# Optimization experiments

Measured on AMD Instinct MI355X. Metric: run time of the kernel, lower is better.

Reference implementation:

```python
import jax, jax.numpy as jnp
import numpy as np

B, H, S, D = 2, 12, 4096, 64
BLK = 64              # from_block_size == to_block_size
NB = S // BLK         # 64 blocks
R = 3                 # num_rand_blocks
NEG = -10000.0


def setup_inputs() -> dict:
    key = jax.random.key(0)
    kq, kk, kv, kr = jax.random.split(key, 4)
    f32 = jnp.float32
    return dict(
        query_layer=jax.random.normal(kq, (B, H, S, D), dtype=f32),
        key_layer=jax.random.normal(kk, (B, H, S, D), dtype=f32),
        value_layer=jax.random.normal(kv, (B, H, S, D), dtype=f32),
        band_mask=jnp.ones((B, 1, NB - 4, BLK, 3 * BLK), dtype=f32),
        from_mask=jnp.ones((B, 1, S, 1), dtype=f32),
        to_mask=jnp.ones((B, 1, 1, S), dtype=f32),
        from_blocked_mask=jnp.ones((B, NB, BLK), dtype=f32),
        to_blocked_mask=jnp.ones((B, NB, BLK), dtype=f32),
        rand_attn=jax.random.randint(kr, (B, H, NB - 2, R), 1, NB - 1, dtype=jnp.int32),
    )


def reference(query_layer, key_layer, value_layer, band_mask, from_mask, to_mask,
              from_blocked_mask, to_blocked_mask, rand_attn):
    b, h, f, d = query_layer.shape
    t = key_layer.shape[2]
    wm = band_mask.shape[3]          # from block size
    wn = band_mask.shape[4] // 3     # to block size
    nf, nt = f // wm, t // wn
    r = rand_attn.shape[-1]
    scale = 1.0 / np.sqrt(d).astype(np.float32)
    softmax = lambda x: jax.nn.softmax(x, axis=-1)

    bq = query_layer.reshape(b, h, nf, wm, d)
    bk = key_layer.reshape(b, h, nt, wn, d)
    bv = value_layer.reshape(b, h, nt, wn, d)

    # gather random key/value blocks: [b,h,nf-2,r*wn,d]
    idx = rand_attn.reshape(b, h, (nf - 2) * r, 1, 1)
    gk = jnp.take_along_axis(bk, idx, axis=2).reshape(b, h, nf - 2, r * wn, d)
    gv = jnp.take_along_axis(bv, idx, axis=2).reshape(b, h, nf - 2, r * wn, d)

    # random attention mask: [b,h,nf-2,wm,r*wn]
    rm = jax.vmap(lambda m, i: m[i])(to_blocked_mask, rand_attn)  # [b,h,nf-2,r,wn]
    rm = rm.reshape(b, h, nf - 2, r * wn)
    rand_mask = jnp.einsum('blq,bhlk->bhlqk', from_blocked_mask[:, 1:-1], rm)

    # --- first query block: dense attention over all keys ---
    fp = jnp.einsum('bhqd,bhkd->bhqk', bq[:, :, 0], key_layer) * scale
    fp = fp + (1.0 - to_mask) * NEG
    first_ctx = jnp.einsum('bhqk,bhkd->bhqd', softmax(fp), value_layer)[:, :, None]

    # --- second query block: blocks 0,1,2, last, random ---
    sk = jnp.concatenate([bk[:, :, 0], bk[:, :, 1], bk[:, :, 2], bk[:, :, -1], gk[:, :, 0]], axis=2)
    sv = jnp.concatenate([bv[:, :, 0], bv[:, :, 1], bv[:, :, 2], bv[:, :, -1], gv[:, :, 0]], axis=2)
    sp = jnp.einsum('bhqd,bhkd->bhqk', bq[:, :, 1], sk) * scale
    seq_pad = jnp.concatenate([to_mask[:, :, :, :3 * wn], to_mask[:, :, :, -wn:],
                               jnp.ones((b, 1, 1, r * wn), dtype=to_mask.dtype)], axis=3)
    rnd_pad = jnp.concatenate([jnp.ones((b, h, wm, 4 * wn), dtype=rand_mask.dtype),
                               rand_mask[:, :, 0]], axis=3)
    sp = sp + (1.0 - jnp.minimum(seq_pad, rnd_pad)) * NEG
    second_ctx = jnp.einsum('bhqk,bhkd->bhqd', softmax(sp), sv)[:, :, None]

    # --- middle blocks: sliding window + random + 2 global ---
    exp_k = jnp.concatenate([bk[:, :, 1:-3], bk[:, :, 2:-2], bk[:, :, 3:-1]], axis=3)
    exp_v = jnp.concatenate([bv[:, :, 1:-3], bv[:, :, 2:-2], bv[:, :, 3:-1]], axis=3)
    mq = bq[:, :, 2:-2]
    inner = jnp.einsum('bhlqd,bhlkd->bhlqk', mq, exp_k) * scale + (1.0 - band_mask) * NEG
    randp = jnp.einsum('bhlqd,bhlkd->bhlqk', mq, gk[:, :, 1:-1]) * scale \
            + (1.0 - rand_mask[:, :, 1:-1]) * NEG
    firstp = jnp.einsum('bhlqd,bhkd->bhlqk', mq, bk[:, :, 0]) * scale \
             + (1.0 - to_mask[:, :, :, :wn][:, :, :, None, :]) * NEG
    lastp = jnp.einsum('bhlqd,bhkd->bhlqk', mq, bk[:, :, -1]) * scale \
            + (1.0 - to_mask[:, :, :, -wn:][:, :, :, None, :]) * NEG
    band = jnp.concatenate([firstp, inner, randp, lastp], axis=-1)
    aw = softmax(band)
    ctx = jnp.einsum('bhlqk,bhlkd->bhlqd', aw[..., wn:4 * wn], exp_v)
    ctx = ctx + jnp.einsum('bhlqk,bhlkd->bhlqd', aw[..., 4 * wn:-wn], gv[:, :, 1:-1])
    ctx = ctx + jnp.einsum('bhlqk,bhkd->bhlqd', aw[..., :wn], bv[:, :, 0])
    ctx = ctx + jnp.einsum('bhlqk,bhkd->bhlqd', aw[..., -wn:], bv[:, :, -1])

    # --- second-to-last query block ---
    slk = jnp.concatenate([bk[:, :, 0], bk[:, :, -3], bk[:, :, -2], bk[:, :, -1], gk[:, :, -1]], axis=2)
    slv = jnp.concatenate([bv[:, :, 0], bv[:, :, -3], bv[:, :, -2], bv[:, :, -1], gv[:, :, -1]], axis=2)
    slp = jnp.einsum('bhqd,bhkd->bhqk', bq[:, :, -2], slk) * scale
    seq_pad2 = jnp.concatenate([to_mask[:, :, :, :wn], to_mask[:, :, :, -3 * wn:],
                                jnp.ones((b, 1, 1, r * wn), dtype=to_mask.dtype)], axis=3)
    rnd_pad2 = jnp.concatenate([jnp.ones((b, h, wm, 4 * wn), dtype=rand_mask.dtype),
                                rand_mask[:, :, -1]], axis=3)
    slp = slp + (1.0 - jnp.minimum(seq_pad2, rnd_pad2)) * NEG
    second_last_ctx = jnp.einsum('bhqk,bhkd->bhqd', softmax(slp), slv)[:, :, None]

    # --- last query block: dense attention over all keys ---
    lp = jnp.einsum('bhqd,bhkd->bhqk', bq[:, :, -1], key_layer) * scale
    lp = lp + (1.0 - to_mask) * NEG
    last_ctx = jnp.einsum('bhqk,bhkd->bhqd', softmax(lp), value_layer)[:, :, None]

    out = jnp.concatenate([first_ctx, second_ctx, ctx, second_last_ctx, last_ctx], axis=2)
    out = out.reshape(b, h, f, d) * from_mask
    return jnp.transpose(out, (0, 2, 1, 3))  # [b, f, h, d]
```

## Files before the change

### kernel.cpp

```cpp
#include <hip/hip_runtime.h>
#include <math.h>

#define PS 4224
#define NEG -10000.f

typedef short short8v __attribute__((ext_vector_type(8)));
typedef float f32x4  __attribute__((ext_vector_type(4)));

#define KHo  0
#define KLo  4096
#define VTHo 8192
#define VTLo 12288
#define LDS_TOT 16384

__device__ __forceinline__ unsigned au(float x){ return __float_as_uint(x); }
__device__ __forceinline__ float    af(unsigned x){ return __uint_as_float(x); }

__device__ __forceinline__ void pack4(float a, float b, float c, float d,
                                      unsigned &h01, unsigned &h23,
                                      unsigned &l01, unsigned &l23) {
    unsigned u0=au(a), u1=au(b), u2=au(c), u3=au(d);
    h01 = __builtin_amdgcn_perm(u1, u0, 0x07060302);
    h23 = __builtin_amdgcn_perm(u3, u2, 0x07060302);
    float r0 = a - af(u0 & 0xffff0000u);
    float r1 = b - af(u1 & 0xffff0000u);
    float r2 = c - af(u2 & 0xffff0000u);
    float r3 = d - af(u3 & 0xffff0000u);
    l01 = __builtin_amdgcn_perm(au(r1), au(r0), 0x07060302);
    l23 = __builtin_amdgcn_perm(au(r3), au(r2), 0x07060302);
}

__device__ __forceinline__ int swz(int row, int colus) {
    return row*64 + (((colus>>3) ^ (row&7))<<3) + (colus&7);
}

#define MFMA(a,b,c) __builtin_amdgcn_mfma_f32_16x16x32_bf16((a),(b),(c),0,0,0)

union FragU { unsigned u[4]; short8v s; };

__device__ __forceinline__ void tile_of(bool partial, bool isMid, int m, int seg,
                                        int r0, int r1, int r2i, int t,
                                        int &blk, int &ty) {
    if (partial)     { blk = seg*8 + t; ty = 0; }
    else if (isMid) {
        if (t == 0)      { blk = 0;       ty = 0; }
        else if (t <= 3) { blk = m-2 + t; ty = t; }
        else if (t <= 6) { blk = (t==4)?r0:((t==5)?r1:r2i); ty = 4; }
        else             { blk = 63;      ty = 0; }
    } else {
        if (t < 4) { blk = (m==1) ? ((t<3)? t : 63) : ((t==0)? 0 : 60+t); ty = 0; }
        else       { blk = (t==4)?r0:((t==5)?r1:r2i); ty = 4; }
    }
}

__global__ __launch_bounds__(256, 3) void bigbird_attn(
    const float* __restrict__ Qg, const float* __restrict__ Kg, const float* __restrict__ Vg,
    const float* __restrict__ band_mask, const float* __restrict__ from_mask,
    const float* __restrict__ to_mask, const float* __restrict__ fbm,
    const float* __restrict__ tbm, const int* __restrict__ rand_attn,
    float* __restrict__ out, float* __restrict__ ws)
{
    const int H = 12, S = 4096;
    __shared__ __align__(16) unsigned short lds[LDS_TOT];

    const int tid  = threadIdx.x;
    const int w    = tid >> 6;
    const int lane = tid & 63;
    const int l15  = lane & 15;
    const int l4   = lane >> 4;

    int wg = blockIdx.x;
    int b, h, m, seg = 0;
    bool partial;
    if (wg < 384) {
        partial = true;
        b = wg / 192;
        int r = wg - b*192;
        h = r >> 4;
        int r2 = r & 15;
        m = (r2 >> 3) ? 63 : 0;
        seg = r2 & 7;
    } else {
        partial = false;
        int ww = wg - 384;
        b = ww / (H*62);
        int r = ww - b*H*62;
        h = r / 62;
        m = 1 + (r - h*62);
    }

    const long bh = (long)b*H + h;
    const float* Qb = Qg + (bh*S + (long)m*64)*64;
    const float* Kb = Kg + bh*S*64;
    const float* Vb = Vg + bh*S*64;

    const bool isMid = (m >= 2) && (m <= 61);
    int nt_cnt;
    int r0 = 1, r1 = 1, r2i = 1;
    if (partial) nt_cnt = 8;
    else {
        const int* ra = rand_attn + (bh*62 + (m-1))*3;
        r0 = ra[0]; r1 = ra[1]; r2i = ra[2];
        nt_cnt = isMid ? 8 : 7;
    }

    short8v qhf[2], qlf[2];
    #pragma unroll
    for (int ks = 0; ks < 2; ++ks) {
        const float* qp = &Qb[(16*w + l15)*64 + l4*8 + 32*ks];
        float4 a = *(const float4*)qp;
        float4 b2 = *(const float4*)(qp + 4);
        FragU fh, fl;
        pack4(a.x,a.y,a.z,a.w, fh.u[0],fh.u[1], fl.u[0],fl.u[1]);
        pack4(b2.x,b2.y,b2.z,b2.w, fh.u[2],fh.u[3], fl.u[2],fl.u[3]);
        qhf[ks] = fh.s; qlf[ks] = fl.s;
    }

    const int kr0 = tid >> 4;
    const int kc  = (tid & 15) << 2;
    const int vd  = tid & 63;
    const int vkg = tid >> 6;

    int blkN, tyN;
    tile_of(partial, isMid, m, seg, r0, r1, r2i, 0, blkN, tyN);
    float4 kreg[4];
    float  vreg[16];
    {
        const float* Kt = Kb + (long)blkN*4096;
        const float* Vt0 = Vb + (long)blkN*4096;
        #pragma unroll
        for (int c = 0; c < 4; ++c) kreg[c] = *(const float4*)&Kt[(kr0+16*c)*64 + kc];
        #pragma unroll
        for (int p = 0; p < 4; ++p)
            #pragma unroll
            for (int i = 0; i < 4; ++i)
                vreg[p*4+i] = Vt0[(p*16 + vkg*4 + i)*64 + vd];
    }

    f32x4 oacc[4];
    #pragma unroll
    for (int i = 0; i < 4; ++i) oacc[i] = (f32x4){0.f,0.f,0.f,0.f};
    float mrow = -INFINITY, lrow = 0.f;

    for (int t = 0; t < nt_cnt; ++t) {
        const int blk = blkN, ty = tyN;

        __syncthreads();

        #pragma unroll
        for (int c = 0; c < 4; ++c) {
            FragU fh, fl;
            pack4(kreg[c].x,kreg[c].y,kreg[c].z,kreg[c].w, fh.u[0],fh.u[1], fl.u[0],fl.u[1]);
            int o = swz(kr0+16*c, kc);
            *(uint2*)&lds[KHo + o] = make_uint2(fh.u[0],fh.u[1]);
            *(uint2*)&lds[KLo + o] = make_uint2(fl.u[0],fl.u[1]);
        }
        #pragma unroll
        for (int p = 0; p < 4; ++p) {
            FragU fh, fl;
            pack4(vreg[p*4+0],vreg[p*4+1],vreg[p*4+2],vreg[p*4+3],
                  fh.u[0],fh.u[1], fl.u[0],fl.u[1]);
            int o = swz(vd, p*16 + vkg*4);
            *(uint2*)&lds[VTHo + o] = make_uint2(fh.u[0],fh.u[1]);
            *(uint2*)&lds[VTLo + o] = make_uint2(fl.u[0],fl.u[1]);
        }
        __syncthreads();

        if (t + 1 < nt_cnt) {
            tile_of(partial, isMid, m, seg, r0, r1, r2i, t+1, blkN, tyN);
            const float* Kt = Kb + (long)blkN*4096;
            const float* Vt0 = Vb + (long)blkN*4096;
            #pragma unroll
            for (int c = 0; c < 4; ++c) kreg[c] = *(const float4*)&Kt[(kr0+16*c)*64 + kc];
            #pragma unroll
            for (int p = 0; p < 4; ++p)
                #pragma unroll
                for (int i = 0; i < 4; ++i)
                    vreg[p*4+i] = Vt0[(p*16 + vkg*4 + i)*64 + vd];
        }

        f32x4 addv[4];
        if (ty == 0) {
            #pragma unroll
            for (int nt = 0; nt < 4; ++nt) {
                f32x4 tv = *(const f32x4*)&to_mask[(long)b*S + blk*64 + 16*nt + 4*l4];
                addv[nt] = (1.f - tv) * NEG;
            }
        } else if (ty <= 3) {
            const float* bq = band_mask + ((long)(b*60 + (m-2)))*64*192
                              + (16*w + l15)*192 + (ty-1)*64;
            #pragma unroll
            for (int nt = 0; nt < 4; ++nt) {
                f32x4 tv = *(const f32x4*)&bq[16*nt + 4*l4];
                addv[nt] = (1.f - tv) * NEG;
            }
        } else {
            float fq = fbm[((long)b*64 + m)*64 + 16*w + l15];
            #pragma unroll
            for (int nt = 0; nt < 4; ++nt) {
                f32x4 tv = *(const f32x4*)&tbm[((long)b*64 + blk)*64 + 16*nt + 4*l4];
                addv[nt] = (1.f - fq*tv) * NEG;
            }
        }

        f32x4 sacc[4];
        #pragma unroll
        for (int nt = 0; nt < 4; ++nt) sacc[nt] = (f32x4){0.f,0.f,0.f,0.f};
        #pragma unroll
        for (int ks = 0; ks < 2; ++ks) {
            const int col = l4*8 + 32*ks;
            #pragma unroll
            for (int nt = 0; nt < 4; ++nt) {
                int o = swz(16*nt + l15, col);
                short8v kh = *(const short8v*)&lds[KHo + o];
                short8v kl = *(const short8v*)&lds[KLo + o];
                sacc[nt] = MFMA(kh, qhf[ks], sacc[nt]);
                sacc[nt] = MFMA(kl, qhf[ks], sacc[nt]);
                sacc[nt] = MFMA(kh, qlf[ks], sacc[nt]);
            }
        }

        f32x4 sr[4];
        float mx = -INFINITY;
        #pragma unroll
        for (int nt = 0; nt < 4; ++nt) {
            sr[nt] = sacc[nt]*0.125f + addv[nt];
            mx = fmaxf(mx, fmaxf(fmaxf(sr[nt][0], sr[nt][1]), fmaxf(sr[nt][2], sr[nt][3])));
        }
        mx = fmaxf(mx, __shfl_xor(mx, 16));
        mx = fmaxf(mx, __shfl_xor(mx, 32));
        float mn = fmaxf(mrow, mx);
        float al = __expf(mrow - mn);
        float ls = 0.f;
        f32x4 pq[4];
        #pragma unroll
        for (int nt = 0; nt < 4; ++nt) {
            pq[nt][0] = __expf(sr[nt][0] - mn);
            pq[nt][1] = __expf(sr[nt][1] - mn);
            pq[nt][2] = __expf(sr[nt][2] - mn);
            pq[nt][3] = __expf(sr[nt][3] - mn);
            ls += pq[nt][0] + pq[nt][1] + pq[nt][2] + pq[nt][3];
        }
        ls += __shfl_xor(ls, 16);
        ls += __shfl_xor(ls, 32);
        lrow = lrow*al + ls;
        mrow = mn;

        unsigned ph01[4], ph23[4], pl01[4], pl23[4];
        #pragma unroll
        for (int nt = 0; nt < 4; ++nt)
            pack4(pq[nt][0],pq[nt][1],pq[nt][2],pq[nt][3],
                  ph01[nt],ph23[nt], pl01[nt],pl23[nt]);

        short8v pbh[2], pbl[2];
        #pragma unroll
        for (int ks = 0; ks < 2; ++ks) {
            const int loNT = 2*ks, hiNT = 2*ks+1;
            const bool up = (l4 & 2);
            unsigned aH0 = up ? ph01[hiNT] : ph01[loNT];
            unsigned aH1 = up ? ph23[hiNT] : ph23[loNT];
            unsigned aL0 = up ? pl01[hiNT] : pl01[loNT];
            unsigned aL1 = up ? pl23[hiNT] : pl23[loNT];
            unsigned sH0 = up ? ph01[loNT] : ph01[hiNT];
            unsigned sH1 = up ? ph23[loNT] : ph23[hiNT];
            unsigned sL0 = up ? pl01[loNT] : pl01[hiNT];
            unsigned sL1 = up ? pl23[loNT] : pl23[hiNT];
            unsigned x16H0 = __shfl_xor((int)aH0, 16), x16H1 = __shfl_xor((int)aH1, 16);
            unsigned x16L0 = __shfl_xor((int)aL0, 16), x16L1 = __shfl_xor((int)aL1, 16);
            unsigned x32H0 = __shfl_xor((int)sH0, 32), x32H1 = __shfl_xor((int)sH1, 32);
            unsigned x32L0 = __shfl_xor((int)sL0, 32), x32L1 = __shfl_xor((int)sL1, 32);
            unsigned x48H0 = __shfl_xor((int)sH0, 48), x48H1 = __shfl_xor((int)sH1, 48);
            unsigned x48L0 = __shfl_xor((int)sL0, 48), x48L1 = __shfl_xor((int)sL1, 48);
            FragU fh, fl;
            fh.u[0] = (l4==0)?aH0 : (l4==1)?x48H0 : (l4==2)?x32H0 : x16H0;
            fh.u[1] = (l4==0)?aH1 : (l4==1)?x48H1 : (l4==2)?x32H1 : x16H1;
            fh.u[2] = (l4==0)?x16H0 : (l4==1)?x32H0 : (l4==2)?x48H0 : aH0;
            fh.u[3] = (l4==0)?x16H1 : (l4==1)?x32H1 : (l4==2)?x48H1 : aH1;
            fl.u[0] = (l4==0)?aL0 : (l4==1)?x48L0 : (l4==2)?x32L0 : x16L0;
            fl.u[1] = (l4==0)?aL1 : (l4==1)?x48L1 : (l4==2)?x32L1 : x16L1;
            fl.u[2] = (l4==0)?x16L0 : (l4==1)?x32L0 : (l4==2)?x48L0 : aL0;
            fl.u[3] = (l4==0)?x16L1 : (l4==1)?x32L1 : (l4==2)?x48L1 : aL1;
            pbh[ks] = fh.s; pbl[ks] = fl.s;
        }

        #pragma unroll
        for (int dnt = 0; dnt < 4; ++dnt) oacc[dnt] *= al;
        #pragma unroll
        for (int ks = 0; ks < 2; ++ks) {
            const int col = l4*8 + 32*ks;
            #pragma unroll
            for (int dnt = 0; dnt < 4; ++dnt) {
                int o = swz(16*dnt + l15, col);
                short8v vh = *(const short8v*)&lds[VTHo + o];
                short8v vl = *(const short8v*)&lds[VTLo + o];
                oacc[dnt] = MFMA(vh, pbh[ks], oacc[dnt]);
                oacc[dnt] = MFMA(vl, pbh[ks], oacc[dnt]);
                oacc[dnt] = MFMA(vh, pbl[ks], oacc[dnt]);
            }
        }
    }

    const int q64 = 16*w + l15;
    if (partial) {
        float* P = ws + ((bh*2 + (m ? 1 : 0))*8 + seg) * PS;
        #pragma unroll
        for (int dnt = 0; dnt < 4; ++dnt)
            *(f32x4*)&P[q64*64 + 16*dnt + 4*l4] = oacc[dnt];
        if (l4 == 0) { P[4096 + q64] = mrow; P[4160 + q64] = lrow; }
    } else {
        int qg = m*64 + q64;
        float scn = (1.f / lrow) * from_mask[(long)b*S + qg];
        #pragma unroll
        for (int dnt = 0; dnt < 4; ++dnt) {
            f32x4 o = oacc[dnt] * scn;
            *(f32x4*)&out[((long)((long)b*S + qg)*H + h)*64 + 16*dnt + 4*l4] = o;
        }
    }
}

__global__ __launch_bounds__(256) void bigbird_reduce(
    const float* __restrict__ ws, const float* __restrict__ from_mask,
    float* __restrict__ out)
{
    const int H = 12, S = 4096;
    int rowIdx = blockIdx.x;
    int b  = rowIdx / 24;
    int r  = rowIdx - b*24;
    int h  = r >> 1;
    int mi = r & 1;
    int m  = mi ? 63 : 0;

    const float* base = ws + (long)rowIdx * 8 * PS;
    int tid = threadIdx.x;
    int q  = tid >> 2;
    int dd = (tid & 3) << 4;

    float msg[8], lsg[8];
    float M = -INFINITY;
    #pragma unroll
    for (int s = 0; s < 8; ++s) {
        msg[s] = base[s*PS + 4096 + q];
        lsg[s] = base[s*PS + 4160 + q];
        M = fmaxf(M, msg[s]);
    }
    float L = 0.f, wv[8];
    #pragma unroll
    for (int s = 0; s < 8; ++s) { wv[s] = __expf(msg[s] - M); L += wv[s]*lsg[s]; }

    int qg = m*64 + q;
    float sc = from_mask[(long)b*S + qg] / L;

    #pragma unroll
    for (int c = 0; c < 4; ++c) {
        float4 o = make_float4(0.f, 0.f, 0.f, 0.f);
        #pragma unroll
        for (int s = 0; s < 8; ++s) {
            float4 a = *(const float4*)&base[s*PS + q*64 + dd + 4*c];
            o.x += wv[s]*a.x; o.y += wv[s]*a.y; o.z += wv[s]*a.z; o.w += wv[s]*a.w;
        }
        o.x *= sc; o.y *= sc; o.z *= sc; o.w *= sc;
        *(float4*)&out[((long)((long)b*S + qg)*H + h)*64 + dd + 4*c] = o;
    }
}

extern "C" void kernel_launch(void* const* d_in, const int* in_sizes, int n_in,
                              void* d_out, int out_size, void* d_ws, size_t ws_size,
                              hipStream_t stream) {
    const float* q   = (const float*)d_in[0];
    const float* k   = (const float*)d_in[1];
    const float* v   = (const float*)d_in[2];
    const float* bm  = (const float*)d_in[3];
    const float* fm  = (const float*)d_in[4];
    const float* tm  = (const float*)d_in[5];
    const float* fbm = (const float*)d_in[6];
    const float* tbm = (const float*)d_in[7];
    const int*   ra  = (const int*)d_in[8];
    float* out = (float*)d_out;
    float* ws  = (float*)d_ws;

    bigbird_attn<<<dim3(384 + 2*12*62), dim3(256), 0, stream>>>(q, k, v, bm, fm, tm, fbm, tbm, ra, out, ws);
    bigbird_reduce<<<dim3(48), dim3(256), 0, stream>>>(ws, fm, out);
}
```

Baseline: 201.5 us.

## Fuse split-KV reduction into attention kernel via last-block atomic counter

Removes the separate reduce kernel. The last of the 8 partial workgroups for each first or last query block now merges the partial softmax results, detected with an atomic counter after a threadfence, and the counters are zeroed by a memset before launch. The block index is remapped so each head's 78 tiles are spread across the 8 XCDs in an interleaved order, and launch bounds are raised to 4 waves per SIMD. This saves one kernel launch and the tail of the reduce, at the cost of a memset, atomics, and possible register pressure from the higher occupancy target.

Result: slower. 285.3 us (+41.6%).

```diff
diff --git a/kernel.cpp b/kernel.cpp
--- a/kernel.cpp
+++ b/kernel.cpp
@@ -2,6 +2,7 @@
 #include <math.h>
 
 #define PS 4224
+#define CNT_OFF 1622016
 #define NEG -10000.f
 
 typedef short short8v __attribute__((ext_vector_type(8)));
@@ -53,7 +54,7 @@
     }
 }
 
-__global__ __launch_bounds__(256, 3) void bigbird_attn(
+__global__ __launch_bounds__(256, 4) void bigbird_attn(
     const float* __restrict__ Qg, const float* __restrict__ Kg, const float* __restrict__ Vg,
     const float* __restrict__ band_mask, const float* __restrict__ from_mask,
     const float* __restrict__ to_mask, const float* __restrict__ fbm,
@@ -62,6 +63,7 @@
 {
     const int H = 12, S = 4096;
     __shared__ __align__(16) unsigned short lds[LDS_TOT];
+    __shared__ int lastFlag;
 
     const int tid  = threadIdx.x;
     const int w    = tid >> 6;
@@ -69,25 +71,15 @@
     const int l15  = lane & 15;
     const int l4   = lane >> 4;
 
-    int wg = blockIdx.x;
-    int b, h, m, seg = 0;
+    int wg0 = blockIdx.x;
+    int u   = (wg0 & 7) * 234 + (wg0 >> 3);
+    int head = u / 78;
+    int within = u - head*78;
+    int b = head / 12, h = head - (head/12)*12;
+    int m, seg = 0;
     bool partial;
-    if (wg < 384) {
-        partial = true;
-        b = wg / 192;
-        int r = wg - b*192;
-        h = r >> 4;
-        int r2 = r & 15;
-        m = (r2 >> 3) ? 63 : 0;
-        seg = r2 & 7;
-    } else {
-        partial = false;
-        int ww = wg - 384;
-        b = ww / (H*62);
-        int r = ww - b*H*62;
-        h = r / 62;
-        m = 1 + (r - h*62);
-    }
+    if (within < 16) { partial = true;  m = (within >= 8) ? 63 : 0; seg = within & 7; }
+    else             { partial = false; m = within - 15; }
 
     const long bh = (long)b*H + h;
     const float* Qb = Qg + (bh*S + (long)m*64)*64;
@@ -302,11 +294,50 @@
 
     const int q64 = 16*w + l15;
     if (partial) {
-        float* P = ws + ((bh*2 + (m ? 1 : 0))*8 + seg) * PS;
+        const int rowIdx = (int)(bh*2 + (m ? 1 : 0));
+        float* P = ws + ((long)rowIdx*8 + seg) * PS;
         #pragma unroll
         for (int dnt = 0; dnt < 4; ++dnt)
             *(f32x4*)&P[q64*64 + 16*dnt + 4*l4] = oacc[dnt];
         if (l4 == 0) { P[4096 + q64] = mrow; P[4160 + q64] = lrow; }
+
+        __threadfence();
+        if (tid == 0) {
+            int* cnt = (int*)(ws + CNT_OFF);
+            int old = atomicAdd(&cnt[rowIdx], 1);
+            lastFlag = (old == 7);
+        }
+        __syncthreads();
+        if (lastFlag) {
+            __threadfence();
+            const float* base = ws + (long)rowIdx * 8 * PS;
+            int q  = tid >> 2;
+            int dd = (tid & 3) << 4;
+            float msg[8], lsg[8];
+            float M = -INFINITY;
+            #pragma unroll
+            for (int s = 0; s < 8; ++s) {
+                msg[s] = base[s*PS + 4096 + q];
+                lsg[s] = base[s*PS + 4160 + q];
+                M = fmaxf(M, msg[s]);
+            }
+            float L = 0.f, wv[8];
+            #pragma unroll
+            for (int s = 0; s < 8; ++s) { wv[s] = __expf(msg[s] - M); L += wv[s]*lsg[s]; }
+            int qg = m*64 + q;
+            float sc = from_mask[(long)b*S + qg] / L;
+            #pragma unroll
+            for (int c = 0; c < 4; ++c) {
+                float4 o = make_float4(0.f, 0.f, 0.f, 0.f);
+                #pragma unroll
+                for (int s = 0; s < 8; ++s) {
+                    float4 a = *(const float4*)&base[s*PS + q*64 + dd + 4*c];
+                    o.x += wv[s]*a.x; o.y += wv[s]*a.y; o.z += wv[s]*a.z; o.w += wv[s]*a.w;
+                }
+                o.x *= sc; o.y *= sc; o.z *= sc; o.w *= sc;
+                *(float4*)&out[((long)((long)b*S + qg)*H + h)*64 + dd + 4*c] = o;
+            }
+        }
     } else {
         int qg = m*64 + q64;
         float scn = (1.f / lrow) * from_mask[(long)b*S + qg];
@@ -315,51 +346,6 @@
             f32x4 o = oacc[dnt] * scn;
             *(f32x4*)&out[((long)((long)b*S + qg)*H + h)*64 + 16*dnt + 4*l4] = o;
         }
-    }
-}
-
-__global__ __launch_bounds__(256) void bigbird_reduce(
-    const float* __restrict__ ws, const float* __restrict__ from_mask,
-    float* __restrict__ out)
-{
-    const int H = 12, S = 4096;
-    int rowIdx = blockIdx.x;
-    int b  = rowIdx / 24;
-    int r  = rowIdx - b*24;
-    int h  = r >> 1;
-    int mi = r & 1;
-    int m  = mi ? 63 : 0;
-
-    const float* base = ws + (long)rowIdx * 8 * PS;
-    int tid = threadIdx.x;
-    int q  = tid >> 2;
-    int dd = (tid & 3) << 4;
-
-    float msg[8], lsg[8];
-    float M = -INFINITY;
-    #pragma unroll
-    for (int s = 0; s < 8; ++s) {
-        msg[s] = base[s*PS + 4096 + q];
-        lsg[s] = base[s*PS + 4160 + q];
-        M = fmaxf(M, msg[s]);
-    }
-    float L = 0.f, wv[8];
-    #pragma unroll
-    for (int s = 0; s < 8; ++s) { wv[s] = __expf(msg[s] - M); L += wv[s]*lsg[s]; }
-
-    int qg = m*64 + q;
-    float sc = from_mask[(long)b*S + qg] / L;
-
-    #pragma unroll
-    for (int c = 0; c < 4; ++c) {
-        float4 o = make_float4(0.f, 0.f, 0.f, 0.f);
-        #pragma unroll
-        for (int s = 0; s < 8; ++s) {
-            float4 a = *(const float4*)&base[s*PS + q*64 + dd + 4*c];
-            o.x += wv[s]*a.x; o.y += wv[s]*a.y; o.z += wv[s]*a.z; o.w += wv[s]*a.w;
-        }
-        o.x *= sc; o.y *= sc; o.z *= sc; o.w *= sc;
-        *(float4*)&out[((long)((long)b*S + qg)*H + h)*64 + dd + 4*c] = o;
     }
 }
 
@@ -378,6 +364,6 @@
     float* out = (float*)d_out;
     float* ws  = (float*)d_ws;
 
-    bigbird_attn<<<dim3(384 + 2*12*62), dim3(256), 0, stream>>>(q, k, v, bm, fm, tm, fbm, tbm, ra, out, ws);
-    bigbird_reduce<<<dim3(48), dim3(256), 0, stream>>>(ws, fm, out);
-}
+    hipMemsetAsync((char*)d_ws + (size_t)CNT_OFF*4, 0, 48*sizeof(int), stream);
+    bigbird_attn<<<dim3(1872), dim3(256), 0, stream>>>(q, k, v, bm, fm, tm, fbm, tbm, ra, out, ws);
+}
```
